# Kernel tuning notes

Measured on AMD Instinct MI355X. Metric: run time of the kernel, lower is better.

Reference implementation:

```python
import jax, jax.numpy as jnp
import numpy as np
import math

S, B, D_MODEL = 1024, 2, 1024
N_HEADS = 16
D_HEAD = D_MODEL // N_HEADS
C = 32  # compressed_len


def _xavier(key, shape):
    fan_in, fan_out = shape[-1], shape[-2] if len(shape) > 1 else shape[-1]
    limit = math.sqrt(6.0 / (fan_in + fan_out))
    return jax.random.uniform(key, shape, jnp.float32, -limit, limit)


def setup_inputs() -> dict:
    key = jax.random.key(0)
    ks = jax.random.split(key, 10)
    return {
        "x": jax.random.normal(ks[0], (S, B, D_MODEL), jnp.float32),
        "q_down": _xavier(ks[1], (C, D_MODEL)),
        "Wq": _xavier(ks[2], (D_MODEL, D_MODEL)),
        "bq": jnp.zeros((D_MODEL,), jnp.float32),
        "Wk": _xavier(ks[3], (D_MODEL, D_MODEL)),
        "bk": jnp.zeros((D_MODEL,), jnp.float32),
        "Wv": _xavier(ks[4], (D_MODEL, D_MODEL)),
        "bv": jnp.zeros((D_MODEL,), jnp.float32),
        "Wo": _xavier(ks[5], (D_MODEL, D_MODEL)),
        "bo": jnp.zeros((D_MODEL,), jnp.float32),
    }


def reference(x, q_down, Wq, bq, Wk, bk, Wv, bv, Wo, bo):
    # x: (s, b, d_model); causal=True, rope=None, dropout inactive (eval)
    s, b, d_model = x.shape
    h, dh = N_HEADS, D_HEAD
    scale = 1.0 / math.sqrt(dh)

    q_u = x @ Wq.T + bq                       # (s,b,dm)
    k_d = x @ Wk.T + bk
    v_d = x @ Wv.T + bv
    v_d_k = v_d @ Wk.T + bk
    v_d_v = v_d @ Wv.T + bv

    def heads(t):  # (s,b,dm) -> (b,h,s,dh)
        return t.reshape(s, b, h, dh).transpose(1, 2, 0, 3)

    q_u = heads(q_u) * scale
    k_d = heads(k_d)
    v_d_kv = jnp.concatenate([heads(v_d_k), heads(v_d_v)], axis=-1)  # (b,h,s,2dh)

    q_d = q_down.reshape(C, h, dh).transpose(1, 0, 2) * scale        # (h,c,dh)

    down = jnp.einsum('hcd,bhsd->bhcs', q_d, k_d)                    # (b,h,c,s)
    w = jnp.exp(down - jnp.max(down, axis=-1, keepdims=True))
    norm = jnp.cumsum(w, axis=-1)

    # (b,h,c,s,2dh): running compressed KV state
    kv_u = jnp.cumsum(w[..., None] * v_d_kv[:, :, None, :, :], axis=3) / norm[..., None]
    k_u, v_u = jnp.split(kv_u, 2, axis=-1)                           # each (b,h,c,s,dh)

    up = jnp.einsum('bhsd,bhcsd->bhsc', q_u, k_u)
    up = jax.nn.softmax(up, axis=-1)
    out = jnp.einsum('bhsc,bhcsd->bhsd', up, v_u)                    # (b,h,s,dh)

    out = out.transpose(2, 0, 1, 3).reshape(s, b, d_model)
    return out @ Wo.T + bo
```

## Files before the change

### kernel.cpp

```cpp
#include <hip/hip_runtime.h>
#include <cstdint>
#include <cstddef>

#define S_LEN 1024
#define BATCH 2
#define DM    1024
#define NH    16
#define DH    64
#define CC    32
#define SB    2048
#define TSD   128
#define NCHD  8

using short8 = __attribute__((ext_vector_type(8))) short;
using f32x4  = __attribute__((ext_vector_type(4))) float;

__device__ __forceinline__ float b2f(unsigned short u) {
    union { unsigned int i; float f; } v; v.i = ((unsigned int)u) << 16; return v.f;
}
__device__ __forceinline__ unsigned short f2b(float f) {
    union { float f; unsigned int i; } v; v.f = f;
    unsigned int x = v.i;
    unsigned int r = x + 0x7FFFu + ((x >> 16) & 1u);
    return (unsigned short)(r >> 16);
}

__device__ __forceinline__ void async_ld16(const unsigned short* g, unsigned short* l) {
    __builtin_amdgcn_global_load_lds(
        (const __attribute__((address_space(1))) unsigned int*)g,
        (__attribute__((address_space(3))) unsigned int*)l,
        16, 0, 0);
}

__global__ __launch_bounds__(256) void k_convert(
    const void* x, const void* qd,
    const void* wq, const void* wk, const void* wv, const void* wo,
    const void* bq, const void* bk, const void* bv, const void* bo,
    int* __restrict__ flag,
    unsigned short* xb, unsigned short* qdb,
    unsigned short* Wqb, unsigned short* Wkb, unsigned short* Wvb, unsigned short* Wob,
    float* biasf)
{
    __shared__ int cnt;
    if (threadIdx.x == 0) cnt = 0;
    __syncthreads();
    {
        const unsigned short* xs = (const unsigned short*)x;
        int local = 0;
        for (int i = threadIdx.x; i < 1024; i += 256) {
            unsigned e = (xs[i * 2] >> 7) & 0xFF;
            if (e >= 90 && e <= 160) local++;
        }
        atomicAdd(&cnt, local);
    }
    __syncthreads();
    const int isbf = (cnt >= 640);
    if (blockIdx.x == 0 && threadIdx.x == 0) *flag = isbf;

    const size_t tid = (size_t)blockIdx.x * 256 + threadIdx.x;
    const size_t stride = (size_t)gridDim.x * 256;

    if (!isbf) {
        auto cv = [&](const void* src, unsigned short* dst, size_t n) {
            const float4* s = (const float4*)src;
            for (size_t i = tid; i < n / 4; i += stride) {
                float4 v = s[i];
                ushort4 o;
                o.x = f2b(v.x); o.y = f2b(v.y); o.z = f2b(v.z); o.w = f2b(v.w);
                ((ushort4*)dst)[i] = o;
            }
        };
        cv(x,  xb,  (size_t)SB * DM);
        cv(qd, qdb, (size_t)CC * DM);
        cv(wq, Wqb, (size_t)DM * DM);
        cv(wk, Wkb, (size_t)DM * DM);
        cv(wv, Wvb, (size_t)DM * DM);
        cv(wo, Wob, (size_t)DM * DM);
    }
    for (size_t i = tid; i < 5 * DM; i += stride) {
        int w = (int)(i >> 10), o = (int)(i & 1023);
        float val;
        if (w == 4) val = 0.f;
        else {
            const void* bp = (w == 0) ? bq : ((w == 1) ? bk : ((w == 2) ? bv : bo));
            val = isbf ? b2f(((const unsigned short*)bp)[o]) : ((const float*)bp)[o];
        }
        biasf[i] = val;
    }
}

struct GArg {
    const unsigned short* A0;
    const unsigned short* A1;
    const unsigned short* B0;
    const unsigned short* B1;
    const float* bias;
    void* out;
    float scale;
    int mode;
};

__global__ __launch_bounds__(256) void gemm_bt(GArg g0, GArg g1, GArg g2, GArg g3,
                                               const int* __restrict__ flag,
                                               int M, int N, int K)
{
    GArg ga = (blockIdx.z == 0) ? g0 : (blockIdx.z == 1) ? g1 : (blockIdx.z == 2) ? g2 : g3;
    const int isbf = *flag;
    const unsigned short* Ap = isbf ? ga.A1 : ga.A0;
    const unsigned short* Bp = isbf ? ga.B1 : ga.B0;
    const int m0 = blockIdx.y * 128;
    const int n0 = blockIdx.x * 128;
    __shared__ __align__(16) unsigned short As[2][128 * 32];
    __shared__ __align__(16) unsigned short Bs[2][128 * 32];
    const int t = threadIdx.x;
    const int w = t >> 6, l = t & 63;
    const int wy = w >> 1, wx = w & 1;
    const int lr = l >> 2;
    const int lk = (l & 3) * 8;
    const int ln = l & 15;
    const int lq = l >> 4;

    f32x4 acc[4][4] = {};

    const unsigned short* Ab0 = Ap + (size_t)(m0 + w * 32 +      lr) * K + lk;
    const unsigned short* Ab1 = Ap + (size_t)(m0 + w * 32 + 16 + lr) * K + lk;
    const unsigned short* Bb0 = Bp + (size_t)(n0 + w * 32 +      lr) * K + lk;
    const unsigned short* Bb1 = Bp + (size_t)(n0 + w * 32 + 16 + lr) * K + lk;

    for (int kk = 0; kk < K; kk += 64) {
#pragma unroll
        for (int hh = 0; hh < 2; ++hh) {
            async_ld16(Ab0 + kk + hh * 32, &As[hh][w * 1024]);
            async_ld16(Ab1 + kk + hh * 32, &As[hh][w * 1024 + 512]);
            async_ld16(Bb0 + kk + hh * 32, &Bs[hh][w * 1024]);
            async_ld16(Bb1 + kk + hh * 32, &Bs[hh][w * 1024 + 512]);
        }
        __syncthreads();
#pragma unroll
        for (int hh = 0; hh < 2; ++hh) {
            short8 af[4], bfr[4];
#pragma unroll
            for (int i = 0; i < 4; ++i)
                af[i] = *(const short8*)&As[hh][(wy * 64 + i * 16 + ln) * 32 + lq * 8];
#pragma unroll
            for (int j = 0; j < 4; ++j)
                bfr[j] = *(const short8*)&Bs[hh][(wx * 64 + j * 16 + ln) * 32 + lq * 8];
#pragma unroll
            for (int i = 0; i < 4; ++i)
#pragma unroll
                for (int j = 0; j < 4; ++j)
                    acc[i][j] = __builtin_amdgcn_mfma_f32_16x16x32_bf16(af[i], bfr[j], acc[i][j], 0, 0, 0);
        }
        __syncthreads();
    }

    const int f32o = (ga.mode == 0) ? 1 : (ga.mode == 1) ? 0 : (!isbf);
    const float sc = ga.scale;
#pragma unroll
    for (int j = 0; j < 4; ++j) {
        int col = n0 + wx * 64 + j * 16 + ln;
        float bv = ga.bias[col];
#pragma unroll
        for (int i = 0; i < 4; ++i) {
            int row0 = m0 + wy * 64 + i * 16 + lq * 4;
#pragma unroll
            for (int r = 0; r < 4; ++r) {
                float v = (acc[i][j][r] + bv) * sc;
                size_t idx = (size_t)(row0 + r) * N + col;
                if (f32o) ((float*)ga.out)[idx] = v;
                else      ((unsigned short*)ga.out)[idx] = f2b(v);
            }
        }
    }
}

__global__ __launch_bounds__(256) void gemm_bt_n64(GArg g0, GArg g1,
                                                   const int* __restrict__ flag,
                                                   int M, int N, int K)
{
    GArg ga = (blockIdx.z == 0) ? g0 : g1;
    const int isbf = *flag;
    const unsigned short* Ap = isbf ? ga.A1 : ga.A0;
    const unsigned short* Bp = isbf ? ga.B1 : ga.B0;
    const int m0 = blockIdx.y * 128;
    const int n0 = blockIdx.x * 64;
    __shared__ __align__(16) unsigned short As[2][128 * 32];
    __shared__ __align__(16) unsigned short Bs[2][64 * 32];
    const int t = threadIdx.x;
    const int w = t >> 6, l = t & 63;
    const int wy = w >> 1, wx = w & 1;
    const int lr = l >> 2;
    const int lk = (l & 3) * 8;
    const int ln = l & 15;
    const int lq = l >> 4;

    f32x4 acc[4][2] = {};

    const unsigned short* Ab0 = Ap + (size_t)(m0 + w * 32 +      lr) * K + lk;
    const unsigned short* Ab1 = Ap + (size_t)(m0 + w * 32 + 16 + lr) * K + lk;
    const unsigned short* Bb  = Bp + (size_t)(n0 + w * 16 + lr) * K + lk;

    for (int kk = 0; kk < K; kk += 64) {
#pragma unroll
        for (int hh = 0; hh < 2; ++hh) {
            async_ld16(Ab0 + kk + hh * 32, &As[hh][w * 1024]);
            async_ld16(Ab1 + kk + hh * 32, &As[hh][w * 1024 + 512]);
            async_ld16(Bb  + kk + hh * 32, &Bs[hh][w * 512]);
        }
        __syncthreads();
#pragma unroll
        for (int hh = 0; hh < 2; ++hh) {
            short8 af[4], bfr[2];
#pragma unroll
            for (int i = 0; i < 4; ++i)
                af[i] = *(const short8*)&As[hh][(wy * 64 + i * 16 + ln) * 32 + lq * 8];
#pragma unroll
            for (int j = 0; j < 2; ++j)
                bfr[j] = *(const short8*)&Bs[hh][(wx * 32 + j * 16 + ln) * 32 + lq * 8];
#pragma unroll
            for (int i = 0; i < 4; ++i)
#pragma unroll
                for (int j = 0; j < 2; ++j)
                    acc[i][j] = __builtin_amdgcn_mfma_f32_16x16x32_bf16(af[i], bfr[j], acc[i][j], 0, 0, 0);
        }
        __syncthreads();
    }

    const int f32o = (ga.mode == 0) ? 1 : (ga.mode == 1) ? 0 : (!isbf);
    const float sc = ga.scale;
#pragma unroll
    for (int j = 0; j < 2; ++j) {
        int col = n0 + wx * 32 + j * 16 + ln;
        float bv = ga.bias[col];
#pragma unroll
        for (int i = 0; i < 4; ++i) {
            int row0 = m0 + wy * 64 + i * 16 + lq * 4;
#pragma unroll
            for (int r = 0; r < 4; ++r) {
                float v = (acc[i][j][r] + bv) * sc;
                size_t idx = (size_t)(row0 + r) * N + col;
                if (f32o) ((float*)ga.out)[idx] = v;
                else      ((unsigned short*)ga.out)[idx] = f2b(v);
            }
        }
    }
}

__global__ __launch_bounds__(256) void k_g2down(
    GArg g0, GArg g1, const int* __restrict__ flag, int M, int N, int K,
    const unsigned short* __restrict__ kd,
    const unsigned short* __restrict__ qd0,
    const unsigned short* __restrict__ qd1,
    float* __restrict__ wbuf,
    float* __restrict__ cmax,
    float* __restrict__ csum)
{
    __shared__ __align__(16) unsigned char SM[40448];
    const int isbf = *flag;
    const int t = threadIdx.x;
    const int w = t >> 6, l = t & 63;
    const int ln = l & 15, lq = l >> 4;

    if (blockIdx.z < 2) {
        unsigned short* As = (unsigned short*)SM;
        unsigned short* Bs = (unsigned short*)(SM + 16384);
        GArg ga = blockIdx.z ? g1 : g0;
        const unsigned short* Ap = isbf ? ga.A1 : ga.A0;
        const unsigned short* Bp = isbf ? ga.B1 : ga.B0;
        const int m0 = blockIdx.y * 128;
        const int n0 = blockIdx.x * 128;
        const int wy = w >> 1, wx = w & 1;
        const int lr = l >> 2;
        const int lk = (l & 3) * 8;

        f32x4 acc[4][4] = {};

        const unsigned short* Ab0 = Ap + (size_t)(m0 + w * 32 +      lr) * K + lk;
        const unsigned short* Ab1 = Ap + (size_t)(m0 + w * 32 + 16 + lr) * K + lk;
        const unsigned short* Bb0 = Bp + (size_t)(n0 + w * 32 +      lr) * K + lk;
        const unsigned short* Bb1 = Bp + (size_t)(n0 + w * 32 + 16 + lr) * K + lk;

        for (int kk = 0; kk < K; kk += 64) {
#pragma unroll
            for (int hh = 0; hh < 2; ++hh) {
                async_ld16(Ab0 + kk + hh * 32, &As[hh * 4096 + w * 1024]);
                async_ld16(Ab1 + kk + hh * 32, &As[hh * 4096 + w * 1024 + 512]);
                async_ld16(Bb0 + kk + hh * 32, &Bs[hh * 4096 + w * 1024]);
                async_ld16(Bb1 + kk + hh * 32, &Bs[hh * 4096 + w * 1024 + 512]);
            }
            __syncthreads();
#pragma unroll
            for (int hh = 0; hh < 2; ++hh) {
                short8 af[4], bfr[4];
#pragma unroll
                for (int i = 0; i < 4; ++i)
                    af[i] = *(const short8*)&As[hh * 4096 + (wy * 64 + i * 16 + ln) * 32 + lq * 8];
#pragma unroll
                for (int j = 0; j < 4; ++j)
                    bfr[j] = *(const short8*)&Bs[hh * 4096 + (wx * 64 + j * 16 + ln) * 32 + lq * 8];
#pragma unroll
                for (int i = 0; i < 4; ++i)
#pragma unroll
                    for (int j = 0; j < 4; ++j)
                        acc[i][j] = __builtin_amdgcn_mfma_f32_16x16x32_bf16(af[i], bfr[j], acc[i][j], 0, 0, 0);
            }
            __syncthreads();
        }

        const int f32o = (ga.mode == 0) ? 1 : (ga.mode == 1) ? 0 : (!isbf);
        const float sc = ga.scale;
#pragma unroll
        for (int j = 0; j < 4; ++j) {
            int col = n0 + wx * 64 + j * 16 + ln;
            float bv = ga.bias[col];
#pragma unroll
            for (int i = 0; i < 4; ++i) {
                int row0 = m0 + wy * 64 + i * 16 + lq * 4;
#pragma unroll
                for (int r = 0; r < 4; ++r) {
                    float v = (acc[i][j][r] + bv) * sc;
                    size_t idx = (size_t)(row0 + r) * N + col;
                    if (f32o) ((float*)ga.out)[idx] = v;
                    else      ((unsigned short*)ga.out)[idx] = f2b(v);
                }
            }
        }
    } else {
        unsigned short* QD = (unsigned short*)SM;
        unsigned short* KT = (unsigned short*)(SM + 4608);
        float* SS          = (float*)(SM + 23040);
        float* cmf         = (float*)(SM + 39936);

        const int id = (blockIdx.z - 2) * 128 + blockIdx.y * 8 + blockIdx.x;
        const unsigned short* qdw = isbf ? qd1 : qd0;
        const int bh = id >> 3;
        const int b = bh >> 4, h = bh & 15;
        const int chunk = id & 7;
        const int s0 = chunk * TSD;

        {
            int r = t >> 3, cb = (t & 7) * 8;
            *(short8*)&QD[r * 72 + cb] = *(const short8*)&qdw[(size_t)r * DM + h * DH + cb];
        }
        for (int u = t; u < 128 * 8; u += 256) {
            int r = u >> 3, cb = (u & 7) * 8;
            *(short8*)&KT[r * 72 + cb] =
                *(const short8*)&kd[(size_t)((s0 + r) * BATCH + b) * DM + h * DH + cb];
        }
        __syncthreads();

        f32x4 accG[2][2] = {};
#pragma unroll
        for (int ks = 0; ks < 2; ++ks) {
            short8 a8[2], b8[2];
#pragma unroll
            for (int i = 0; i < 2; ++i)
                a8[i] = *(const short8*)&QD[(i * 16 + ln) * 72 + ks * 32 + lq * 8];
#pragma unroll
            for (int j = 0; j < 2; ++j)
                b8[j] = *(const short8*)&KT[(w * 32 + j * 16 + ln) * 72 + ks * 32 + lq * 8];
#pragma unroll
            for (int i = 0; i < 2; ++i)
#pragma unroll
                for (int j = 0; j < 2; ++j)
                    accG[i][j] = __builtin_amdgcn_mfma_f32_16x16x32_bf16(a8[i], b8[j], accG[i][j], 0, 0, 0);
        }
#pragma unroll
        for (int i = 0; i < 2; ++i) {
#pragma unroll
            for (int j = 0; j < 2; ++j) {
                int sl = w * 32 + j * 16 + ln;
#pragma unroll
                for (int r = 0; r < 4; ++r) {
                    int c = i * 16 + lq * 4 + r;
                    float v = accG[i][j][r] * 0.125f;
                    SS[c * 132 + sl] = v;
                    wbuf[((size_t)bh * CC + c) * S_LEN + s0 + sl] = v;
                }
            }
        }
        __syncthreads();

        const int c = t >> 3, sub = t & 7;
        float lmax = -3.4e38f;
#pragma unroll
        for (int k = 0; k < 16; ++k) lmax = fmaxf(lmax, SS[c * 132 + sub * 16 + k]);
        lmax = fmaxf(lmax, __shfl_xor(lmax, 1));
        lmax = fmaxf(lmax, __shfl_xor(lmax, 2));
        lmax = fmaxf(lmax, __shfl_xor(lmax, 4));
        if (sub == 0) {
            cmf[c] = lmax;
            cmax[((size_t)bh * CC + c) * NCHD + chunk] = lmax;
        }
        __syncthreads();
        const float cm = cmf[c];
        float es = 0.f;
#pragma unroll
        for (int k = 0; k < 16; ++k) es += __expf(SS[c * 132 + sub * 16 + k] - cm);
        es += __shfl_xor(es, 1);
        es += __shfl_xor(es, 2);
        es += __shfl_xor(es, 4);
        if (sub == 0) csum[((size_t)bh * CC + c) * NCHD + chunk] = es;
    }
}

__global__ __launch_bounds__(256) void k_wapply(const float* __restrict__ wbuf,
                                                const float* __restrict__ cmax,
                                                const float* __restrict__ csum,
                                                unsigned short* __restrict__ wb,
                                                unsigned short* __restrict__ wT,
                                                float* __restrict__ invn)
{
    const int bh = blockIdx.x, seg = blockIdx.y;
    const int t = threadIdx.x;
    __shared__ float gm[CC];
    __shared__ float basep[CC];
    __shared__ float psum[CC][9];
    __shared__ unsigned short wTt[128 * 40];
    __shared__ float invt[128 * 36];

    if (t < CC) {
        const size_t cb = (size_t)(bh * CC + t) * NCHD;
        float m = cmax[cb];
#pragma unroll
        for (int g = 1; g < NCHD; ++g) m = fmaxf(m, cmax[cb + g]);
        gm[t] = m;
        float bsum = 0.f;
        for (int k = 0; k < seg; ++k)
            bsum += csum[cb + k] * __expf(cmax[cb + k] - m);
        basep[t] = bsum;
    }
    __syncthreads();

    const int c = t >> 3, sub = t & 7;
    const float gmc = gm[c];
    const size_t rbase = (size_t)bh * 32768 + c * 1024 + seg * 128 + sub * 16;
    float w16[16];
    float s = 0.f;
#pragma unroll
    for (int i = 0; i < 16; ++i) {
        float v = __expf(wbuf[rbase + i] - gmc);
        w16[i] = v; s += v;
    }
    psum[c][sub] = s;
    short8 o0, o1;
#pragma unroll
    for (int i = 0; i < 8; ++i) { o0[i] = f2b(w16[i]); o1[i] = f2b(w16[8 + i]); }
    *(short8*)&wb[rbase] = o0;
    *(short8*)&wb[rbase + 8] = o1;
#pragma unroll
    for (int i = 0; i < 16; ++i) wTt[(sub * 16 + i) * 40 + c] = f2b(w16[i]);
    __syncthreads();

    float run = basep[c];
    for (int k = 0; k < sub; ++k) run += psum[c][k];
#pragma unroll
    for (int i = 0; i < 16; ++i) {
        run += w16[i];
        invt[(sub * 16 + i) * 36 + c] = 1.0f / fmaxf(run, 1e-30f);
    }
    __syncthreads();

    for (int u = t; u < 128 * 4; u += 256) {
        int r = u >> 2, cb = (u & 3) * 8;
        *(short8*)&wT[(size_t)bh * 32768 + (seg * 128 + r) * 32 + cb] =
            *(const short8*)&wTt[r * 40 + cb];
    }
    for (int u = t; u < 128 * 8; u += 256) {
        int r = u >> 3, cb = (u & 7) * 4;
        *(float4*)&invn[(size_t)bh * 32768 + (seg * 128 + r) * 32 + cb] =
            *(const float4*)&invt[r * 36 + cb];
    }
}

__global__ __launch_bounds__(256) void k_state(const unsigned short* __restrict__ wb,
                                               const unsigned short* __restrict__ vdk,
                                               const unsigned short* __restrict__ vdv,
                                               float* __restrict__ Mst,
                                               float* __restrict__ NTst)
{
    const int bh = blockIdx.x, ch = blockIdx.y;
    const int b = bh >> 4, h = bh & 15;
    const int s0 = ch * 64;
    const int t = threadIdx.x;
    const int w = t >> 6, l = t & 63;
    const int ln = l & 15, lq = l >> 4;
    __shared__ __align__(16) unsigned short Ws[32 * 72];
    __shared__ __align__(16) unsigned short T1[64 * 72];
    __shared__ __align__(16) unsigned short T2[64 * 72];
    __shared__ __align__(16) unsigned short KT[64 * 72];
    __shared__ __align__(16) unsigned short VT[64 * 72];

    for (int u = t; u < 32 * 8; u += 256) {
        int r = u >> 3, cb = (u & 7) * 8;
        *(short8*)&Ws[r * 72 + cb] = *(const short8*)&wb[(size_t)bh * 32768 + r * 1024 + s0 + cb];
    }
    for (int u = t; u < 64 * 8; u += 256) {
        int r = u >> 3, cb = (u & 7) * 8;
        *(short8*)&T1[r * 72 + cb] =
            *(const short8*)&vdk[(size_t)((s0 + r) * BATCH + b) * DM + h * DH + cb];
        *(short8*)&T2[r * 72 + cb] =
            *(const short8*)&vdv[(size_t)((s0 + r) * BATCH + b) * DM + h * DH + cb];
    }
    __syncthreads();
    for (int u = t; u < 64 * 8; u += 256) {
        int d = u >> 3, s8 = (u & 7) * 8;
        short8 o1, o2;
#pragma unroll
        for (int k = 0; k < 8; ++k) {
            o1[k] = T1[(s8 + k) * 72 + d];
            o2[k] = T2[(s8 + k) * 72 + d];
        }
        *(short8*)&KT[d * 72 + s8] = o1;
        *(short8*)&VT[d * 72 + s8] = o2;
    }
    __syncthreads();

    f32x4 accM[2] = {};
#pragma unroll
    for (int ks = 0; ks < 2; ++ks) {
        short8 b8 = *(const short8*)&KT[(w * 16 + ln) * 72 + ks * 32 + lq * 8];
#pragma unroll
        for (int i = 0; i < 2; ++i) {
            short8 a8 = *(const short8*)&Ws[(i * 16 + ln) * 72 + ks * 32 + lq * 8];
            accM[i] = __builtin_amdgcn_mfma_f32_16x16x32_bf16(a8, b8, accM[i], 0, 0, 0);
        }
    }
#pragma unroll
    for (int i = 0; i < 2; ++i)
#pragma unroll
        for (int r = 0; r < 4; ++r)
            Mst[((size_t)(bh * 16 + ch) * 32 + i * 16 + lq * 4 + r) * 64 + w * 16 + ln] = accM[i][r];

    f32x4 accN[2] = {};
#pragma unroll
    for (int ks = 0; ks < 2; ++ks) {
        short8 a8 = *(const short8*)&VT[(w * 16 + ln) * 72 + ks * 32 + lq * 8];
#pragma unroll
        for (int j = 0; j < 2; ++j) {
            short8 b8 = *(const short8*)&Ws[(j * 16 + ln) * 72 + ks * 32 + lq * 8];
            accN[j] = __builtin_amdgcn_mfma_f32_16x16x32_bf16(a8, b8, accN[j], 0, 0, 0);
        }
    }
#pragma unroll
    for (int j = 0; j < 2; ++j)
#pragma unroll
        for (int r = 0; r < 4; ++r)
            NTst[((size_t)(bh * 16 + ch) * 64 + w * 16 + lq * 4 + r) * 32 + j * 16 + ln] = accN[j][r];
}

__global__ __launch_bounds__(256) void k_prefix(const float* __restrict__ Mst,
                                                const float* __restrict__ NTst,
                                                unsigned short* __restrict__ Mcum,
                                                unsigned short* __restrict__ NTcum)
{
    const int bh = blockIdx.x;
    const float* src = blockIdx.y ? NTst : Mst;
    unsigned short* dst = blockIdx.y ? NTcum : Mcum;
    const int e0 = blockIdx.z * 512 + threadIdx.x * 2;
    float r0 = 0.f, r1 = 0.f;
#pragma unroll
    for (int ch = 0; ch < 16; ++ch) {
        size_t off = (size_t)(bh * 16 + ch) * 2048 + e0;
        ushort2 ob; ob.x = f2b(r0); ob.y = f2b(r1);
        *(ushort2*)&dst[off] = ob;
        float2 v = *(const float2*)&src[off];
        r0 += v.x; r1 += v.y;
    }
}

__global__ __launch_bounds__(256) void k_att(
    const unsigned short* __restrict__ qu,
    const unsigned short* __restrict__ vdk,
    const unsigned short* __restrict__ wb,
    const float* __restrict__ invn,
    const unsigned short* __restrict__ wT,
    const unsigned short* __restrict__ vdv,
    const unsigned short* __restrict__ Mcum,
    const unsigned short* __restrict__ NTcum,
    unsigned short* __restrict__ attout)
{
    const int bh = blockIdx.x, b = bh >> 4, h = bh & 15;
    const int qi = blockIdx.y;
    const int s0 = qi * 64;
    const int t = threadIdx.x;
    const int w = t >> 6, l = t & 63;
    const int wy = w >> 1, wx = w & 1;
    const int ln = l & 15, lq = l >> 4;

    __shared__ __align__(16) unsigned short Qs[64 * 72];
    __shared__ __align__(16) unsigned short Gs[64 * 72];
    __shared__ __align__(16) unsigned short Kd[64 * 72];
    __shared__ __align__(16) unsigned short Wd[32 * 72];
    __shared__ __align__(16) unsigned short WTd[64 * 40];
    __shared__ __align__(16) unsigned short VTd[64 * 72];
    __shared__ __align__(16) unsigned short Mc[32 * 72];
    __shared__ __align__(16) unsigned short Nc[64 * 40];

    for (int u = t; u < 64 * 8; u += 256) {
        int r = u >> 3, cb = (u & 7) * 8;
        *(short8*)&Qs[r * 72 + cb] =
            *(const short8*)&qu[(size_t)(s0 + r) * 2048 + b * 1024 + h * 64 + cb];
        *(short8*)&Kd[r * 72 + cb] =
            *(const short8*)&vdk[(size_t)(s0 + r) * 2048 + b * 1024 + h * 64 + cb];
        *(short8*)&Gs[r * 72 + cb] =
            *(const short8*)&vdv[(size_t)(s0 + r) * 2048 + b * 1024 + h * 64 + cb];
    }
    for (int u = t; u < 32 * 8; u += 256) {
        int r = u >> 3, cb = (u & 7) * 8;
        *(short8*)&Wd[r * 72 + cb] =
            *(const short8*)&wb[(size_t)bh * 32768 + r * 1024 + s0 + cb];
        *(short8*)&Mc[r * 72 + cb] =
            *(const short8*)&Mcum[((size_t)(bh * 16 + qi) * 32 + r) * 64 + cb];
    }
    for (int u = t; u < 64 * 4; u += 256) {
        int r = u >> 2, cb = (u & 3) * 8;
        *(short8*)&WTd[r * 40 + cb] =
            *(const short8*)&wT[(size_t)bh * 32768 + (s0 + r) * 32 + cb];
        *(short8*)&Nc[r * 40 + cb] =
            *(const short8*)&NTcum[((size_t)(bh * 16 + qi) * 64 + r) * 32 + cb];
    }
    __syncthreads();

    for (int u = t; u < 64 * 8; u += 256) {
        int d = u >> 3, s8 = (u & 7) * 8;
        short8 o;
#pragma unroll
        for (int k = 0; k < 8; ++k) o[k] = Gs[(s8 + k) * 72 + d];
        *(short8*)&VTd[d * 72 + s8] = o;
    }
    __syncthreads();

    {
        f32x4 accG[2][2] = {};
#pragma unroll
        for (int ks = 0; ks < 2; ++ks) {
            short8 a8[2], b8[2];
#pragma unroll
            for (int i = 0; i < 2; ++i)
                a8[i] = *(const short8*)&Qs[(wy * 32 + i * 16 + ln) * 72 + ks * 32 + lq * 8];
#pragma unroll
            for (int j = 0; j < 2; ++j)
                b8[j] = *(const short8*)&Kd[(wx * 32 + j * 16 + ln) * 72 + ks * 32 + lq * 8];
#pragma unroll
            for (int i = 0; i < 2; ++i)
#pragma unroll
                for (int j = 0; j < 2; ++j)
                    accG[i][j] = __builtin_amdgcn_mfma_f32_16x16x32_bf16(a8[i], b8[j], accG[i][j], 0, 0, 0);
        }
        __syncthreads();
#pragma unroll
        for (int i = 0; i < 2; ++i) {
            int row = wy * 32 + i * 16 + lq * 4;
#pragma unroll
            for (int j = 0; j < 2; ++j) {
                int col = wx * 32 + j * 16 + ln;
#pragma unroll
                for (int r = 0; r < 4; ++r) {
                    float v = accG[i][j][r];
                    if (col > row + r) v = 0.f;
                    Gs[(row + r) * 72 + col] = f2b(v);
                }
            }
        }
    }
    __syncthreads();

    f32x4 accU[2] = {};
#pragma unroll
    for (int ks = 0; ks < 2; ++ks) {
        short8 ga = *(const short8*)&Gs[(w * 16 + ln) * 72 + ks * 32 + lq * 8];
        short8 qa = *(const short8*)&Qs[(w * 16 + ln) * 72 + ks * 32 + lq * 8];
#pragma unroll
        for (int j = 0; j < 2; ++j) {
            short8 wf = *(const short8*)&Wd[(j * 16 + ln) * 72 + ks * 32 + lq * 8];
            short8 mf = *(const short8*)&Mc[(j * 16 + ln) * 72 + ks * 32 + lq * 8];
            accU[j] = __builtin_amdgcn_mfma_f32_16x16x32_bf16(ga, wf, accU[j], 0, 0, 0);
            accU[j] = __builtin_amdgcn_mfma_f32_16x16x32_bf16(qa, mf, accU[j], 0, 0, 0);
        }
    }
    __syncthreads();

    {
        int rowl = w * 16 + lq * 4;
#pragma unroll
        for (int r = 0; r < 4; ++r) {
            int srow = s0 + rowl + r;
            float inv0 = invn[(size_t)bh * 32768 + srow * 32 + ln];
            float inv1 = invn[(size_t)bh * 32768 + srow * 32 + 16 + ln];
            float l0 = accU[0][r] * inv0;
            float l1 = accU[1][r] * inv1;
            float m = fmaxf(l0, l1);
#pragma unroll
            for (int msk = 1; msk < 16; msk <<= 1) m = fmaxf(m, __shfl_xor(m, msk));
            float e0 = __expf(l0 - m), e1 = __expf(l1 - m);
            float Z = e0 + e1;
#pragma unroll
            for (int msk = 1; msk < 16; msk <<= 1) Z += __shfl_xor(Z, msk);
            float iz = 1.0f / Z;
            Qs[(rowl + r) * 40 + ln]      = f2b(e0 * iz * inv0);
            Qs[(rowl + r) * 40 + 16 + ln] = f2b(e1 * iz * inv1);
        }
    }
    __syncthreads();

    short8 pa[2];
#pragma unroll
    for (int i = 0; i < 2; ++i)
        pa[i] = *(const short8*)&Qs[(wy * 32 + i * 16 + ln) * 40 + lq * 8];
    {
        f32x4 accS[2][2] = {};
        short8 b8[2];
#pragma unroll
        for (int j = 0; j < 2; ++j)
            b8[j] = *(const short8*)&WTd[(wx * 32 + j * 16 + ln) * 40 + lq * 8];
#pragma unroll
        for (int i = 0; i < 2; ++i)
#pragma unroll
            for (int j = 0; j < 2; ++j)
                accS[i][j] = __builtin_amdgcn_mfma_f32_16x16x32_bf16(pa[i], b8[j], accS[i][j], 0, 0, 0);
#pragma unroll
        for (int i = 0; i < 2; ++i) {
            int row = wy * 32 + i * 16 + lq * 4;
#pragma unroll
            for (int j = 0; j < 2; ++j) {
                int col = wx * 32 + j * 16 + ln;
#pragma unroll
                for (int r = 0; r < 4; ++r) {
                    float v = accS[i][j][r];
                    if (col > row + r) v = 0.f;
                    Gs[(row + r) * 72 + col] = f2b(v);
                }
            }
        }
    }
    __syncthreads();

    {
        f32x4 accO[2][2] = {};
        short8 n8[2];
#pragma unroll
        for (int j = 0; j < 2; ++j)
            n8[j] = *(const short8*)&Nc[(wx * 32 + j * 16 + ln) * 40 + lq * 8];
#pragma unroll
        for (int i = 0; i < 2; ++i)
#pragma unroll
            for (int j = 0; j < 2; ++j)
                accO[i][j] = __builtin_amdgcn_mfma_f32_16x16x32_bf16(pa[i], n8[j], accO[i][j], 0, 0, 0);
#pragma unroll
        for (int ks = 0; ks < 2; ++ks) {
            short8 a8[2], b8[2];
#pragma unroll
            for (int i = 0; i < 2; ++i)
                a8[i] = *(const short8*)&Gs[(wy * 32 + i * 16 + ln) * 72 + ks * 32 + lq * 8];
#pragma unroll
            for (int j = 0; j < 2; ++j)
                b8[j] = *(const short8*)&VTd[(wx * 32 + j * 16 + ln) * 72 + ks * 32 + lq * 8];
#pragma unroll
            for (int i = 0; i < 2; ++i)
#pragma unroll
                for (int j = 0; j < 2; ++j)
                    accO[i][j] = __builtin_amdgcn_mfma_f32_16x16x32_bf16(a8[i], b8[j], accO[i][j], 0, 0, 0);
        }
#pragma unroll
        for (int i = 0; i < 2; ++i) {
            int rowb = s0 + wy * 32 + i * 16 + lq * 4;
#pragma unroll
            for (int j = 0; j < 2; ++j) {
                int d = wx * 32 + j * 16 + ln;
#pragma unroll
                for (int r = 0; r < 4; ++r)
                    attout[(size_t)(rowb + r) * 2048 + b * 1024 + h * 64 + d] = f2b(accO[i][j][r]);
            }
        }
    }
}

extern "C" void kernel_launch(void* const* d_in, const int* in_sizes, int n_in,
                              void* d_out, int out_size, void* d_ws, size_t ws_size,
                              hipStream_t stream)
{
    (void)in_sizes; (void)n_in; (void)out_size; (void)ws_size;
    char* ws = (char*)d_ws;
    const size_t MB = (size_t)1 << 20;
    const size_t KB = (size_t)1 << 10;
    unsigned short* attout = (unsigned short*)(ws + 0 * MB);
    unsigned short* q_u    = (unsigned short*)(ws + 4 * MB);
    unsigned short* k_d    = (unsigned short*)(ws + 8 * MB);
    unsigned short* v_dk   = (unsigned short*)(ws + 12 * MB);
    unsigned short* v_dv   = (unsigned short*)(ws + 16 * MB);
    float* wbuf = (float*)(ws + 20 * MB);
    unsigned short* wb  = (unsigned short*)(ws + 24 * MB);
    unsigned short* wT  = (unsigned short*)(ws + 26 * MB);
    float* invn = (float*)(ws + 28 * MB);
    float* Mst  = (float*)(ws + 32 * MB);
    float* NTst = (float*)(ws + 36 * MB);
    unsigned short* Mcum  = (unsigned short*)(ws + 40 * MB);
    unsigned short* NTcum = (unsigned short*)(ws + 42 * MB);
    unsigned short* xb  = (unsigned short*)(ws + 44 * MB);
    unsigned short* Wqb = (unsigned short*)(ws + 48 * MB);
    unsigned short* Wkb = (unsigned short*)(ws + 50 * MB);
    unsigned short* Wvb = (unsigned short*)(ws + 52 * MB);
    unsigned short* Wob = (unsigned short*)(ws + 54 * MB);
    unsigned short* v_d = (unsigned short*)(ws + 56 * MB);
    unsigned short* qdb = (unsigned short*)(ws + 62 * MB);
    float* biasf  = (float*)(ws + 62 * MB + 64 * KB);
    float* cmax   = (float*)(ws + 62 * MB + 192 * KB);
    float* csum   = (float*)(ws + 62 * MB + 256 * KB);
    int*   flag   = (int*)  (ws + 62 * MB + 320 * KB);

    const unsigned short* xraw  = (const unsigned short*)d_in[0];
    const unsigned short* qdraw = (const unsigned short*)d_in[1];
    const unsigned short* wqraw = (const unsigned short*)d_in[2];
    const unsigned short* wkraw = (const unsigned short*)d_in[4];
    const unsigned short* wvraw = (const unsigned short*)d_in[6];
    const unsigned short* woraw = (const unsigned short*)d_in[8];

    k_convert<<<1024, 256, 0, stream>>>(
        d_in[0], d_in[1], d_in[2], d_in[4], d_in[6], d_in[8],
        d_in[3], d_in[5], d_in[7], d_in[9],
        flag, xb, qdb, Wqb, Wkb, Wvb, Wob, biasf);

    const float* bqf = biasf;
    const float* bkf = biasf + 1024;
    const float* bvf = biasf + 2048;
    const float* bof = biasf + 3072;

    GArg gq { xb, xraw, Wqb, wqraw, bqf, (void*)q_u, 0.125f, 1 };
    GArg gk { xb, xraw, Wkb, wkraw, bkf, (void*)k_d, 1.0f, 1 };
    GArg gv { xb, xraw, Wvb, wvraw, bvf, (void*)v_d, 1.0f, 1 };
    gemm_bt<<<dim3(8, 16, 3), 256, 0, stream>>>(gq, gk, gv, gq, flag, SB, DM, DM);

    GArg gvk{ v_d, v_d, Wkb, wkraw, bkf, (void*)v_dk, 1.0f, 1 };
    GArg gvv{ v_d, v_d, Wvb, wvraw, bvf, (void*)v_dv, 1.0f, 1 };
    k_g2down<<<dim3(8, 16, 4), 256, 0, stream>>>(gvk, gvv, flag, SB, DM, DM,
                                                 k_d, qdb, qdraw, wbuf, cmax, csum);

    k_wapply<<<dim3(32, 8), 256, 0, stream>>>(wbuf, cmax, csum, wb, wT, invn);
    k_state<<<dim3(32, 16), 256, 0, stream>>>(wb, v_dk, v_dv, Mst, NTst);
    k_prefix<<<dim3(32, 2, 4), 256, 0, stream>>>(Mst, NTst, Mcum, NTcum);
    k_att<<<dim3(32, 16), 256, 0, stream>>>(q_u, v_dk, wb, invn, wT, v_dv, Mcum, NTcum, attout);

    GArg go{ attout, attout, Wob, woraw, bof, d_out, 1.0f, 2 };
    gemm_bt_n64<<<dim3(16, 16, 1), 256, 0, stream>>>(go, go, flag, SB, DM, DM);
}
```

Baseline: 184.8 us.

## Fuse weight-apply with chunk state kernel and fold prefix sum into attention

Merges k_wapply and k_state into one kernel that keeps the exponentiated weights in shared memory and computes per-chunk M/N state for two 64-row chunks per block. The separate k_prefix kernel is removed. k_att now sums the preceding chunk states from fp32 directly. This cuts two kernel launches and the round trip of the weights and cumulative state through global memory. In exchange, k_state runs on half as many blocks (256 instead of 512) with more serial work each, and k_att does a redundant serial prefix over up to 15 chunks per block.

```diff
diff --git a/kernel.cpp b/kernel.cpp
--- a/kernel.cpp
+++ b/kernel.cpp
@@ -404,20 +404,36 @@
     }
 }
 
-__global__ __launch_bounds__(256) void k_wapply(const float* __restrict__ wbuf,
-                                                const float* __restrict__ cmax,
-                                                const float* __restrict__ csum,
-                                                unsigned short* __restrict__ wb,
-                                                unsigned short* __restrict__ wT,
-                                                float* __restrict__ invn)
+__global__ __launch_bounds__(256) void k_wstate(
+    const float* __restrict__ wbuf,
+    const float* __restrict__ cmax,
+    const float* __restrict__ csum,
+    const unsigned short* __restrict__ vdk,
+    const unsigned short* __restrict__ vdv,
+    unsigned short* __restrict__ wb,
+    unsigned short* __restrict__ wT,
+    float* __restrict__ invn,
+    float* __restrict__ Mst,
+    float* __restrict__ NTst)
 {
+    __shared__ __align__(16) unsigned char SM[45568];
+    unsigned short* Wfull = (unsigned short*)SM;
+    unsigned char* R = SM + 8704;
+    float* gm    = (float*)R;
+    float* basep = (float*)(R + 128);
+    float* psum  = (float*)(R + 256);
+    unsigned short* wTt = (unsigned short*)(R + 1408);
+    float* invt  = (float*)(R + 11648);
+    unsigned short* T1 = (unsigned short*)R;
+    unsigned short* T2 = (unsigned short*)(R + 9216);
+    unsigned short* KT = (unsigned short*)(R + 18432);
+    unsigned short* VT = (unsigned short*)(R + 27648);
+
     const int bh = blockIdx.x, seg = blockIdx.y;
+    const int b = bh >> 4, h = bh & 15;
     const int t = threadIdx.x;
-    __shared__ float gm[CC];
-    __shared__ float basep[CC];
-    __shared__ float psum[CC][9];
-    __shared__ unsigned short wTt[128 * 40];
-    __shared__ float invt[128 * 36];
+    const int w = t >> 6, l = t & 63;
+    const int ln = l & 15, lq = l >> 4;
 
     if (t < CC) {
         const size_t cb = (size_t)(bh * CC + t) * NCHD;
@@ -432,140 +448,108 @@
     }
     __syncthreads();
 
-    const int c = t >> 3, sub = t & 7;
-    const float gmc = gm[c];
-    const size_t rbase = (size_t)bh * 32768 + c * 1024 + seg * 128 + sub * 16;
-    float w16[16];
-    float s = 0.f;
-#pragma unroll
-    for (int i = 0; i < 16; ++i) {
-        float v = __expf(wbuf[rbase + i] - gmc);
-        w16[i] = v; s += v;
-    }
-    psum[c][sub] = s;
-    short8 o0, o1;
-#pragma unroll
-    for (int i = 0; i < 8; ++i) { o0[i] = f2b(w16[i]); o1[i] = f2b(w16[8 + i]); }
-    *(short8*)&wb[rbase] = o0;
-    *(short8*)&wb[rbase + 8] = o1;
-#pragma unroll
-    for (int i = 0; i < 16; ++i) wTt[(sub * 16 + i) * 40 + c] = f2b(w16[i]);
-    __syncthreads();
-
-    float run = basep[c];
-    for (int k = 0; k < sub; ++k) run += psum[c][k];
-#pragma unroll
-    for (int i = 0; i < 16; ++i) {
-        run += w16[i];
-        invt[(sub * 16 + i) * 36 + c] = 1.0f / fmaxf(run, 1e-30f);
+    {
+        const int c = t >> 3, sub = t & 7;
+        const float gmc = gm[c];
+        const size_t rbase = (size_t)bh * 32768 + c * 1024 + seg * 128 + sub * 16;
+        float w16[16];
+        float s = 0.f;
+#pragma unroll
+        for (int i = 0; i < 16; ++i) {
+            float v = __expf(wbuf[rbase + i] - gmc);
+            w16[i] = v; s += v;
+        }
+        psum[c * 9 + sub] = s;
+        short8 o0, o1;
+#pragma unroll
+        for (int i = 0; i < 8; ++i) { o0[i] = f2b(w16[i]); o1[i] = f2b(w16[8 + i]); }
+        *(short8*)&wb[rbase] = o0;
+        *(short8*)&wb[rbase + 8] = o1;
+        *(short8*)&Wfull[c * 136 + sub * 16] = o0;
+        *(short8*)&Wfull[c * 136 + sub * 16 + 8] = o1;
+#pragma unroll
+        for (int i = 0; i < 16; ++i) wTt[(sub * 16 + i) * 40 + c] = f2b(w16[i]);
+        __syncthreads();
+
+        float run = basep[c];
+        for (int k = 0; k < sub; ++k) run += psum[c * 9 + k];
+#pragma unroll
+        for (int i = 0; i < 16; ++i) {
+            run += w16[i];
+            invt[(sub * 16 + i) * 36 + c] = 1.0f / fmaxf(run, 1e-30f);
+        }
     }
     __syncthreads();
 
     for (int u = t; u < 128 * 4; u += 256) {
-        int r = u >> 2, cb = (u & 3) * 8;
-        *(short8*)&wT[(size_t)bh * 32768 + (seg * 128 + r) * 32 + cb] =
-            *(const short8*)&wTt[r * 40 + cb];
+        int r = u >> 2, cb2 = (u & 3) * 8;
+        *(short8*)&wT[(size_t)bh * 32768 + (seg * 128 + r) * 32 + cb2] =
+            *(const short8*)&wTt[r * 40 + cb2];
     }
     for (int u = t; u < 128 * 8; u += 256) {
-        int r = u >> 3, cb = (u & 7) * 4;
-        *(float4*)&invn[(size_t)bh * 32768 + (seg * 128 + r) * 32 + cb] =
-            *(const float4*)&invt[r * 36 + cb];
-    }
-}
-
-__global__ __launch_bounds__(256) void k_state(const unsigned short* __restrict__ wb,
-                                               const unsigned short* __restrict__ vdk,
-                                               const unsigned short* __restrict__ vdv,
-                                               float* __restrict__ Mst,
-                                               float* __restrict__ NTst)
-{
-    const int bh = blockIdx.x, ch = blockIdx.y;
-    const int b = bh >> 4, h = bh & 15;
-    const int s0 = ch * 64;
-    const int t = threadIdx.x;
-    const int w = t >> 6, l = t & 63;
-    const int ln = l & 15, lq = l >> 4;
-    __shared__ __align__(16) unsigned short Ws[32 * 72];
-    __shared__ __align__(16) unsigned short T1[64 * 72];
-    __shared__ __align__(16) unsigned short T2[64 * 72];
-    __shared__ __align__(16) unsigned short KT[64 * 72];
-    __shared__ __align__(16) unsigned short VT[64 * 72];
-
-    for (int u = t; u < 32 * 8; u += 256) {
-        int r = u >> 3, cb = (u & 7) * 8;
-        *(short8*)&Ws[r * 72 + cb] = *(const short8*)&wb[(size_t)bh * 32768 + r * 1024 + s0 + cb];
-    }
-    for (int u = t; u < 64 * 8; u += 256) {
-        int r = u >> 3, cb = (u & 7) * 8;
-        *(short8*)&T1[r * 72 + cb] =
-            *(const short8*)&vdk[(size_t)((s0 + r) * BATCH + b) * DM + h * DH + cb];
-        *(short8*)&T2[r * 72 + cb] =
-            *(const short8*)&vdv[(size_t)((s0 + r) * BATCH + b) * DM + h * DH + cb];
-    }
-    __syncthreads();
-    for (int u = t; u < 64 * 8; u += 256) {
-        int d = u >> 3, s8 = (u & 7) * 8;
-        short8 o1, o2;
-#pragma unroll
-        for (int k = 0; k < 8; ++k) {
-            o1[k] = T1[(s8 + k) * 72 + d];
-            o2[k] = T2[(s8 + k) * 72 + d];
-        }
-        *(short8*)&KT[d * 72 + s8] = o1;
-        *(short8*)&VT[d * 72 + s8] = o2;
-    }
-    __syncthreads();
-
-    f32x4 accM[2] = {};
-#pragma unroll
-    for (int ks = 0; ks < 2; ++ks) {
-        short8 b8 = *(const short8*)&KT[(w * 16 + ln) * 72 + ks * 32 + lq * 8];
-#pragma unroll
-        for (int i = 0; i < 2; ++i) {
-            short8 a8 = *(const short8*)&Ws[(i * 16 + ln) * 72 + ks * 32 + lq * 8];
-            accM[i] = __builtin_amdgcn_mfma_f32_16x16x32_bf16(a8, b8, accM[i], 0, 0, 0);
-        }
-    }
-#pragma unroll
-    for (int i = 0; i < 2; ++i)
-#pragma unroll
-        for (int r = 0; r < 4; ++r)
-            Mst[((size_t)(bh * 16 + ch) * 32 + i * 16 + lq * 4 + r) * 64 + w * 16 + ln] = accM[i][r];
-
-    f32x4 accN[2] = {};
-#pragma unroll
-    for (int ks = 0; ks < 2; ++ks) {
-        short8 a8 = *(const short8*)&VT[(w * 16 + ln) * 72 + ks * 32 + lq * 8];
-#pragma unroll
-        for (int j = 0; j < 2; ++j) {
-            short8 b8 = *(const short8*)&Ws[(j * 16 + ln) * 72 + ks * 32 + lq * 8];
-            accN[j] = __builtin_amdgcn_mfma_f32_16x16x32_bf16(a8, b8, accN[j], 0, 0, 0);
-        }
-    }
-#pragma unroll
-    for (int j = 0; j < 2; ++j)
-#pragma unroll
-        for (int r = 0; r < 4; ++r)
-            NTst[((size_t)(bh * 16 + ch) * 64 + w * 16 + lq * 4 + r) * 32 + j * 16 + ln] = accN[j][r];
-}
-
-__global__ __launch_bounds__(256) void k_prefix(const float* __restrict__ Mst,
-                                                const float* __restrict__ NTst,
-                                                unsigned short* __restrict__ Mcum,
-                                                unsigned short* __restrict__ NTcum)
-{
-    const int bh = blockIdx.x;
-    const float* src = blockIdx.y ? NTst : Mst;
-    unsigned short* dst = blockIdx.y ? NTcum : Mcum;
-    const int e0 = blockIdx.z * 512 + threadIdx.x * 2;
-    float r0 = 0.f, r1 = 0.f;
-#pragma unroll
-    for (int ch = 0; ch < 16; ++ch) {
-        size_t off = (size_t)(bh * 16 + ch) * 2048 + e0;
-        ushort2 ob; ob.x = f2b(r0); ob.y = f2b(r1);
-        *(ushort2*)&dst[off] = ob;
-        float2 v = *(const float2*)&src[off];
-        r0 += v.x; r1 += v.y;
+        int r = u >> 3, cb2 = (u & 7) * 4;
+        *(float4*)&invn[(size_t)bh * 32768 + (seg * 128 + r) * 32 + cb2] =
+            *(const float4*)&invt[r * 36 + cb2];
+    }
+    __syncthreads();
+
+    for (int rep = 0; rep < 2; ++rep) {
+        const int ch = seg * 2 + rep;
+        const int s0 = ch * 64;
+
+        for (int u = t; u < 64 * 8; u += 256) {
+            int r = u >> 3, cb = (u & 7) * 8;
+            *(short8*)&T1[r * 72 + cb] =
+                *(const short8*)&vdk[(size_t)((s0 + r) * BATCH + b) * DM + h * DH + cb];
+            *(short8*)&T2[r * 72 + cb] =
+                *(const short8*)&vdv[(size_t)((s0 + r) * BATCH + b) * DM + h * DH + cb];
+        }
+        __syncthreads();
+        for (int u = t; u < 64 * 8; u += 256) {
+            int d = u >> 3, s8 = (u & 7) * 8;
+            short8 o1, o2;
+#pragma unroll
+            for (int k = 0; k < 8; ++k) {
+                o1[k] = T1[(s8 + k) * 72 + d];
+                o2[k] = T2[(s8 + k) * 72 + d];
+            }
+            *(short8*)&KT[d * 72 + s8] = o1;
+            *(short8*)&VT[d * 72 + s8] = o2;
+        }
+        __syncthreads();
+
+        f32x4 accM[2] = {};
+#pragma unroll
+        for (int ks = 0; ks < 2; ++ks) {
+            short8 b8 = *(const short8*)&KT[(w * 16 + ln) * 72 + ks * 32 + lq * 8];
+#pragma unroll
+            for (int i = 0; i < 2; ++i) {
+                short8 a8 = *(const short8*)&Wfull[(i * 16 + ln) * 136 + rep * 64 + ks * 32 + lq * 8];
+                accM[i] = __builtin_amdgcn_mfma_f32_16x16x32_bf16(a8, b8, accM[i], 0, 0, 0);
+            }
+        }
+#pragma unroll
+        for (int i = 0; i < 2; ++i)
+#pragma unroll
+            for (int r = 0; r < 4; ++r)
+                Mst[((size_t)(bh * 16 + ch) * 32 + i * 16 + lq * 4 + r) * 64 + w * 16 + ln] = accM[i][r];
+
+        f32x4 accN[2] = {};
+#pragma unroll
+        for (int ks = 0; ks < 2; ++ks) {
+            short8 a8 = *(const short8*)&VT[(w * 16 + ln) * 72 + ks * 32 + lq * 8];
+#pragma unroll
+            for (int j = 0; j < 2; ++j) {
+                short8 b8 = *(const short8*)&Wfull[(j * 16 + ln) * 136 + rep * 64 + ks * 32 + lq * 8];
+                accN[j] = __builtin_amdgcn_mfma_f32_16x16x32_bf16(a8, b8, accN[j], 0, 0, 0);
+            }
+        }
+#pragma unroll
+        for (int j = 0; j < 2; ++j)
+#pragma unroll
+            for (int r = 0; r < 4; ++r)
+                NTst[((size_t)(bh * 16 + ch) * 64 + w * 16 + lq * 4 + r) * 32 + j * 16 + ln] = accN[j][r];
+        __syncthreads();
     }
 }
 
@@ -576,8 +560,8 @@
     const float* __restrict__ invn,
     const unsigned short* __restrict__ wT,
     const unsigned short* __restrict__ vdv,
-    const unsigned short* __restrict__ Mcum,
-    const unsigned short* __restrict__ NTcum,
+    const float* __restrict__ Mst,
+    const float* __restrict__ NTst,
     unsigned short* __restrict__ attout)
 {
     const int bh = blockIdx.x, b = bh >> 4, h = bh & 15;
@@ -610,15 +594,32 @@
         int r = u >> 3, cb = (u & 7) * 8;
         *(short8*)&Wd[r * 72 + cb] =
             *(const short8*)&wb[(size_t)bh * 32768 + r * 1024 + s0 + cb];
-        *(short8*)&Mc[r * 72 + cb] =
-            *(const short8*)&Mcum[((size_t)(bh * 16 + qi) * 32 + r) * 64 + cb];
     }
     for (int u = t; u < 64 * 4; u += 256) {
         int r = u >> 2, cb = (u & 3) * 8;
         *(short8*)&WTd[r * 40 + cb] =
             *(const short8*)&wT[(size_t)bh * 32768 + (s0 + r) * 32 + cb];
-        *(short8*)&Nc[r * 40 + cb] =
-            *(const short8*)&NTcum[((size_t)(bh * 16 + qi) * 64 + r) * 32 + cb];
+    }
+    {
+        float am[8] = {0.f, 0.f, 0.f, 0.f, 0.f, 0.f, 0.f, 0.f};
+        float an[8] = {0.f, 0.f, 0.f, 0.f, 0.f, 0.f, 0.f, 0.f};
+        for (int ch = 0; ch < qi; ++ch) {
+            const float* pm = Mst + ((size_t)(bh * 16 + ch)) * 2048 + t * 8;
+            const float* pn = NTst + ((size_t)(bh * 16 + ch)) * 2048 + t * 8;
+            float4 m0 = *(const float4*)pm;
+            float4 m1 = *(const float4*)(pm + 4);
+            float4 n0 = *(const float4*)pn;
+            float4 n1 = *(const float4*)(pn + 4);
+            am[0] += m0.x; am[1] += m0.y; am[2] += m0.z; am[3] += m0.w;
+            am[4] += m1.x; am[5] += m1.y; am[6] += m1.z; am[7] += m1.w;
+            an[0] += n0.x; an[1] += n0.y; an[2] += n0.z; an[3] += n0.w;
+            an[4] += n1.x; an[5] += n1.y; an[6] += n1.z; an[7] += n1.w;
+        }
+        short8 mo, no;
+#pragma unroll
+        for (int j = 0; j < 8; ++j) { mo[j] = f2b(am[j]); no[j] = f2b(an[j]); }
+        *(short8*)&Mc[(t >> 3) * 72 + (t & 7) * 8] = mo;
+        *(short8*)&Nc[(t >> 2) * 40 + (t & 3) * 8] = no;
     }
     __syncthreads();
 
@@ -795,8 +796,6 @@
     float* invn = (float*)(ws + 28 * MB);
     float* Mst  = (float*)(ws + 32 * MB);
     float* NTst = (float*)(ws + 36 * MB);
-    unsigned short* Mcum  = (unsigned short*)(ws + 40 * MB);
-    unsigned short* NTcum = (unsigned short*)(ws + 42 * MB);
     unsigned short* xb  = (unsigned short*)(ws + 44 * MB);
     unsigned short* Wqb = (unsigned short*)(ws + 48 * MB);
     unsigned short* Wkb = (unsigned short*)(ws + 50 * MB);
@@ -836,10 +835,10 @@
     k_g2down<<<dim3(8, 16, 4), 256, 0, stream>>>(gvk, gvv, flag, SB, DM, DM,
                                                  k_d, qdb, qdraw, wbuf, cmax, csum);
 
-    k_wapply<<<dim3(32, 8), 256, 0, stream>>>(wbuf, cmax, csum, wb, wT, invn);
-    k_state<<<dim3(32, 16), 256, 0, stream>>>(wb, v_dk, v_dv, Mst, NTst);
-    k_prefix<<<dim3(32, 2, 4), 256, 0, stream>>>(Mst, NTst, Mcum, NTcum);
-    k_att<<<dim3(32, 16), 256, 0, stream>>>(q_u, v_dk, wb, invn, wT, v_dv, Mcum, NTcum, attout);
+    k_wstate<<<dim3(32, 8), 256, 0, stream>>>(wbuf, cmax, csum, v_dk, v_dv,
+                                              wb, wT, invn, Mst, NTst);
+    k_att<<<dim3(32, 16), 256, 0, stream>>>(q_u, v_dk, wb, invn, wT, v_dv,
+                                            Mst, NTst, attout);
 
     GArg go{ attout, attout, Wob, woraw, bof, d_out, 1.0f, 2 };
     gemm_bt_n64<<<dim3(16, 16, 1), 256, 0, stream>>>(go, go, flag, SB, DM, DM);
```

Result: no change. 182.4 us (-1.3%).
